# Kernel tuning notes

Hardware: AMD Instinct MI355X
Metric: run time of the kernel (lower is better)

## Reference

```python
import jax, jax.numpy as jnp
import numpy as np

B, T, D, H, FC = 32768, 7, 40, 64, 32


def lstm_layer(x_seq, W_ih, W_hh, b_ih, b_hh):
    # x_seq: [T, B, Din]; weights in PyTorch layout: W_ih [4H, Din], W_hh [4H, H]
    # Precompute the input contribution to all gates outside the scan.
    gx_seq = jnp.einsum('tbd,gd->tbg', x_seq, W_ih) + b_ih + b_hh  # [T, B, 4H]
    h0 = jnp.zeros((x_seq.shape[1], W_hh.shape[1]), x_seq.dtype)
    c0 = jnp.zeros_like(h0)

    def step(carry, gx):
        h, c = carry
        g = gx + h @ W_hh.T                      # [B, 4H]
        i, f, gg, o = jnp.split(g, 4, axis=-1)   # PyTorch gate order: i, f, g, o
        i = jax.nn.sigmoid(i)
        f = jax.nn.sigmoid(f)
        gg = jnp.tanh(gg)
        o = jax.nn.sigmoid(o)
        c = f * c + i * gg
        h = o * jnp.tanh(c)
        return (h, c), h

    (_, _), hs = jax.lax.scan(step, (h0, c0), gx_seq)
    return hs  # [T, B, H]


def setup_inputs() -> dict:
    key = jax.random.key(0)
    ks = jax.random.split(key, 13)
    s_in = 1.0 / np.sqrt(H)
    u = lambda k, shape: jax.random.uniform(k, shape, jnp.float32, -s_in, s_in)
    return {
        'x': jax.random.normal(ks[0], (B, T, D), jnp.float32),
        'W_ih0': u(ks[1], (4 * H, D)),
        'W_hh0': u(ks[2], (4 * H, H)),
        'b_ih0': u(ks[3], (4 * H,)),
        'b_hh0': u(ks[4], (4 * H,)),
        'W_ih1': u(ks[5], (4 * H, H)),
        'W_hh1': u(ks[6], (4 * H, H)),
        'b_ih1': u(ks[7], (4 * H,)),
        'b_hh1': u(ks[8], (4 * H,)),
        'W1': u(ks[9], (FC, H)),
        'b1': u(ks[10], (FC,)),
        'W2': u(ks[11], (1, FC)),
        'b2': u(ks[12], (1,)),
    }


def reference(x, W_ih0, W_hh0, b_ih0, b_hh0, W_ih1, W_hh1, b_ih1, b_hh1, W1, b1, W2, b2):
    xs = jnp.transpose(x, (1, 0, 2))                    # [T, B, D]
    h1 = lstm_layer(xs, W_ih0, W_hh0, b_ih0, b_hh0)     # [T, B, H]
    h2 = lstm_layer(h1, W_ih1, W_hh1, b_ih1, b_hh1)     # [T, B, H]
    last = h2[-1]                                       # out[:, -1, :] -> [B, H]
    # dropout is identity in eval mode
    hid = jax.nn.relu(last @ W1.T + b1)                 # [B, 32]
    return hid @ W2.T + b2                              # [B, 1]
```

## Files before the change

kernel.cpp:

```cpp
#include <hip/hip_runtime.h>

#define TT 7
#define DD 40
#define HH 64
#define RB 128
#define NRT 8
#define NTH 512
#define HS 72
#define XP 44
#define L2E 1.44269504088896340736f

typedef _Float16 f16x8 __attribute__((ext_vector_type(8)));
typedef float f32x4 __attribute__((ext_vector_type(4)));

#define MFMA(acc, a, b) acc = __builtin_amdgcn_mfma_f32_16x16x32_f16(a, b, acc, 0, 0, 0)

__device__ __forceinline__ float fast_rcp(float x) { return __builtin_amdgcn_rcpf(x); }
__device__ __forceinline__ float ex2(float x) { return __builtin_amdgcn_exp2f(x); }

__device__ __forceinline__ float lstm_hc(float a0, float a1, float a2, float a3,
                                         float &c) {
  float A = ex2(-a0);
  float E = ex2(a2);
  float F = ex2(-a1);
  float O = ex2(-a3);
  float igg = (E - 1.f) * fast_rcp((1.f + A) * (1.f + E));
  float fg  = fast_rcp(1.f + F);
  c = fg * c + igg;
  float C = ex2(c * (2.f * L2E));
  return (C - 1.f) * fast_rcp((1.f + O) * (1.f + C));
}

typedef __attribute__((address_space(3))) unsigned lds_u32_t;
typedef const __attribute__((address_space(1))) unsigned glb_u32_t;
__device__ __forceinline__ void gl_lds16(const void* g, void* l) {
  __builtin_amdgcn_global_load_lds((glb_u32_t*)g, (lds_u32_t*)l, 16, 0, 0);
}

__device__ __forceinline__ f16x8 zf() {
  f16x8 r;
  #pragma unroll
  for (int i = 0; i < 8; ++i) r[i] = (_Float16)0.f;
  return r;
}
__device__ __forceinline__ f16x8 cvt8s(const float* p, float s) {
  float4 a = *(const float4*)p, b = *(const float4*)(p + 4);
  f16x8 r;
  r[0] = (_Float16)(a.x * s); r[1] = (_Float16)(a.y * s);
  r[2] = (_Float16)(a.z * s); r[3] = (_Float16)(a.w * s);
  r[4] = (_Float16)(b.x * s); r[5] = (_Float16)(b.y * s);
  r[6] = (_Float16)(b.z * s); r[7] = (_Float16)(b.w * s);
  return r;
}
__device__ __forceinline__ f16x8 cvt8(const float* p) {
  float4 a = *(const float4*)p, b = *(const float4*)(p + 4);
  f16x8 r;
  r[0] = (_Float16)a.x; r[1] = (_Float16)a.y; r[2] = (_Float16)a.z; r[3] = (_Float16)a.w;
  r[4] = (_Float16)b.x; r[5] = (_Float16)b.y; r[6] = (_Float16)b.z; r[7] = (_Float16)b.w;
  return r;
}
__device__ __forceinline__ f16x8 pk8(float4 a, float4 b) {
  f16x8 r;
  auto p0 = __builtin_amdgcn_cvt_pkrtz(a.x, a.y);
  auto p1 = __builtin_amdgcn_cvt_pkrtz(a.z, a.w);
  auto p2 = __builtin_amdgcn_cvt_pkrtz(b.x, b.y);
  auto p3 = __builtin_amdgcn_cvt_pkrtz(b.z, b.w);
  r[0] = p0[0]; r[1] = p0[1]; r[2] = p1[0]; r[3] = p1[1];
  r[4] = p2[0]; r[5] = p2[1]; r[6] = p3[0]; r[7] = p3[1];
  return r;
}

__global__ __launch_bounds__(NTH, 2) void lstm2_r16_kernel(
    const float* __restrict__ x,
    const float* __restrict__ Wih0, const float* __restrict__ Whh0,
    const float* __restrict__ bih0, const float* __restrict__ bhh0,
    const float* __restrict__ Wih1, const float* __restrict__ Whh1,
    const float* __restrict__ bih1, const float* __restrict__ bhh1,
    const float* __restrict__ W1, const float* __restrict__ b1,
    const float* __restrict__ W2, const float* __restrict__ b2,
    float* __restrict__ out)
{
  __shared__ __align__(16) unsigned short s_h[4][RB * HS];
  __shared__ __align__(16) float s_x[2][RB * XP];

  const int tid = threadIdx.x;
  const int l   = tid & 63;
  const int wv  = tid >> 6;
  const bool L0 = (wv < 4);
  const int l15 = l & 15;
  const int lg  = l >> 4;
  const int jj  = (wv & 3) * 16 + l15;
  const int k0l = lg * 8;
  const int blk = blockIdx.x;
  const float* xg = x + (size_t)blk * RB * (TT * DD);

  const int c0 = tid, c1 = 512 + tid, c2 = 1024 + tid;
  const int r0 = c0 / 11, p0 = c0 - r0 * 11;
  const int r1 = c1 / 11, p1 = c1 - r1 * 11;
  const int r2 = c2 / 11, p2 = c2 - r2 * 11;
  const bool v0 = (p0 < 10), v1 = (p1 < 10), v2 = (c2 < 1408) && (p2 < 10);
  const float* xs0 = xg + r0 * (TT * DD) + p0 * 4;
  const float* xs1 = xg + r1 * (TT * DD) + p1 * 4;
  const float* xs2 = xg + r2 * (TT * DD) + p2 * 4;
  const int d0 = wv * 256, d1 = 2048 + wv * 256, d2 = 4096 + wv * 256;

  if (v0) gl_lds16(xs0, &s_x[0][d0]);
  if (v1) gl_lds16(xs1, &s_x[0][d1]);
  if (v2) gl_lds16(xs2, &s_x[0][d2]);

  f16x8 W[16];
  float biasv[4];
  if (L0) {
    #pragma unroll
    for (int g = 0; g < 4; ++g) {
      const float gs = (g == 2) ? 2.f * L2E : L2E;
      int n = g * 64 + jj;
      W[g]      = cvt8s(&Wih0[n * DD + k0l], gs);
      W[4 + g]  = (lg == 0) ? cvt8s(&Wih0[n * DD + 32], gs) : zf();
      W[8 + g]  = cvt8s(&Whh0[n * HH + k0l], gs);
      W[12 + g] = cvt8s(&Whh0[n * HH + 32 + k0l], gs);
      biasv[g] = (bih0[n] + bhh0[n]) * gs;
    }
  } else {
    #pragma unroll
    for (int g = 0; g < 4; ++g) {
      const float gs = (g == 2) ? 2.f * L2E : L2E;
      int n = g * 64 + jj;
      W[g]      = cvt8s(&Wih1[n * HH + k0l], gs);
      W[4 + g]  = cvt8s(&Wih1[n * HH + 32 + k0l], gs);
      W[8 + g]  = cvt8s(&Whh1[n * HH + k0l], gs);
      W[12 + g] = cvt8s(&Whh1[n * HH + 32 + k0l], gs);
      biasv[g] = (bih1[n] + bhh1[n]) * gs;
    }
  }

  float cst[NRT][4];
  #pragma unroll
  for (int rt = 0; rt < NRT; ++rt)
    #pragma unroll
    for (int r = 0; r < 4; ++r) cst[rt][r] = 0.f;

  __syncthreads();

  #pragma unroll 1
  for (int s = 0; s < TT; ++s) {
    if (s) __syncthreads();
    if (s < TT - 1) {
      float* xd = &s_x[(s + 1) & 1][0];
      const int so = (s + 1) * DD;
      if (v0) gl_lds16(xs0 + so, xd + d0);
      if (v1) gl_lds16(xs1 + so, xd + d1);
      if (v2) gl_lds16(xs2 + so, xd + d2);
    }
    const int p1r = (s - 1) & 1;

    if (L0) {
      const float* xb = &s_x[s & 1][0];
      #pragma unroll
      for (int rt = 0; rt < NRT; ++rt) {
        const float* xr = xb + (rt * 16 + l15) * XP;
        f16x8 xh = pk8(*(const float4*)(xr + k0l), *(const float4*)(xr + k0l + 4));
        f16x8 xm = xh;
        if (lg == 0) xm = pk8(*(const float4*)(xr + 32), *(const float4*)(xr + 36));

        f32x4 acc[4];
        #pragma unroll
        for (int g = 0; g < 4; ++g)
          acc[g] = (f32x4){biasv[g], biasv[g], biasv[g], biasv[g]};

        __builtin_amdgcn_s_setprio(1);
        #pragma unroll
        for (int g = 0; g < 4; ++g) MFMA(acc[g], xh, W[g]);
        #pragma unroll
        for (int g = 0; g < 4; ++g) MFMA(acc[g], xm, W[4 + g]);
        if (s) {
          const unsigned short* hp = &s_h[p1r][(rt * 16 + l15) * HS + k0l];
          f16x8 h1a = *(const f16x8*)hp;
          f16x8 h1b = *(const f16x8*)(hp + 32);
          #pragma unroll
          for (int g = 0; g < 4; ++g) MFMA(acc[g], h1a, W[8 + g]);
          #pragma unroll
          for (int g = 0; g < 4; ++g) MFMA(acc[g], h1b, W[12 + g]);
        }
        __builtin_amdgcn_s_setprio(0);

        #pragma unroll
        for (int r = 0; r < 4; ++r) {
          float h = lstm_hc(acc[0][r], acc[1][r], acc[2][r], acc[3][r], cst[rt][r]);
          s_h[s & 1][(rt * 16 + lg * 4 + r) * HS + jj] =
              __builtin_bit_cast(unsigned short, (_Float16)h);
        }
      }
    } else if (s) {
      #pragma unroll
      for (int rt = 0; rt < NRT; ++rt) {
        const unsigned short* hp = &s_h[p1r][(rt * 16 + l15) * HS + k0l];
        f16x8 h1a = *(const f16x8*)hp;
        f16x8 h1b = *(const f16x8*)(hp + 32);

        f32x4 acc[4];
        #pragma unroll
        for (int g = 0; g < 4; ++g)
          acc[g] = (f32x4){biasv[g], biasv[g], biasv[g], biasv[g]};

        __builtin_amdgcn_s_setprio(1);
        #pragma unroll
        for (int g = 0; g < 4; ++g) MFMA(acc[g], h1a, W[g]);
        #pragma unroll
        for (int g = 0; g < 4; ++g) MFMA(acc[g], h1b, W[4 + g]);
        if (s >= 2) {
          const unsigned short* qp = &s_h[2 + (s & 1)][(rt * 16 + l15) * HS + k0l];
          f16x8 q0 = *(const f16x8*)qp;
          f16x8 q1 = *(const f16x8*)(qp + 32);
          #pragma unroll
          for (int g = 0; g < 4; ++g) MFMA(acc[g], q0, W[8 + g]);
          #pragma unroll
          for (int g = 0; g < 4; ++g) MFMA(acc[g], q1, W[12 + g]);
        }
        __builtin_amdgcn_s_setprio(0);

        #pragma unroll
        for (int r = 0; r < 4; ++r) {
          float h = lstm_hc(acc[0][r], acc[1][r], acc[2][r], acc[3][r], cst[rt][r]);
          s_h[2 + p1r][(rt * 16 + lg * 4 + r) * HS + jj] =
              __builtin_bit_cast(unsigned short, (_Float16)h);
        }
      }
    }
  }

  __syncthreads();
  if (!L0) {
    #pragma unroll
    for (int rt = 0; rt < NRT; ++rt) {
      const unsigned short* hp = &s_h[0][(rt * 16 + l15) * HS + k0l];
      f16x8 h1a = *(const f16x8*)hp;
      f16x8 h1b = *(const f16x8*)(hp + 32);
      const unsigned short* qp = &s_h[3][(rt * 16 + l15) * HS + k0l];
      f16x8 q0 = *(const f16x8*)qp;
      f16x8 q1 = *(const f16x8*)(qp + 32);
      f32x4 acc[4];
      #pragma unroll
      for (int g = 0; g < 4; ++g)
        acc[g] = (f32x4){biasv[g], biasv[g], biasv[g], biasv[g]};
      __builtin_amdgcn_s_setprio(1);
      #pragma unroll
      for (int g = 0; g < 4; ++g) MFMA(acc[g], h1a, W[g]);
      #pragma unroll
      for (int g = 0; g < 4; ++g) MFMA(acc[g], h1b, W[4 + g]);
      #pragma unroll
      for (int g = 0; g < 4; ++g) MFMA(acc[g], q0, W[8 + g]);
      #pragma unroll
      for (int g = 0; g < 4; ++g) MFMA(acc[g], q1, W[12 + g]);
      __builtin_amdgcn_s_setprio(0);
      #pragma unroll
      for (int r = 0; r < 4; ++r) {
        float h = lstm_hc(acc[0][r], acc[1][r], acc[2][r], acc[3][r], cst[rt][r]);
        s_h[1][(rt * 16 + lg * 4 + r) * HS + jj] =
            __builtin_bit_cast(unsigned short, (_Float16)h);
      }
    }
  }
  __syncthreads();

  {
    const unsigned short* ap = &s_h[1][(wv * 16 + l15) * HS + k0l];
    f16x8 A0 = *(const f16x8*)ap;
    f16x8 A1 = *(const f16x8*)(ap + 32);
    f16x8 Bf0[2], Bf1[2];
    f32x4 accf[2];
    #pragma unroll
    for (int f = 0; f < 2; ++f) {
      int n = f * 16 + l15;
      Bf0[f] = cvt8(&W1[n * 64 + k0l]);
      Bf1[f] = cvt8(&W1[n * 64 + 32 + k0l]);
      float bb = b1[n];
      accf[f] = (f32x4){bb, bb, bb, bb};
    }
    #pragma unroll
    for (int f = 0; f < 2; ++f) { MFMA(accf[f], A0, Bf0[f]); MFMA(accf[f], A1, Bf1[f]); }
    float* hid = &s_x[0][0];
    #pragma unroll
    for (int f = 0; f < 2; ++f)
      #pragma unroll
      for (int r = 0; r < 4; ++r)
        hid[(wv * 16 + lg * 4 + r) * 36 + f * 16 + l15] = fmaxf(accf[f][r], 0.f);
  }
  __syncthreads();
  if (tid < RB) {
    const float* hid = &s_x[0][0];
    float a = b2[0];
    #pragma unroll
    for (int kq = 0; kq < 8; ++kq) {
      float4 hv = *(const float4*)&hid[tid * 36 + kq * 4];
      float4 wv4 = *(const float4*)&W2[kq * 4];
      a += hv.x * wv4.x + hv.y * wv4.y + hv.z * wv4.z + hv.w * wv4.w;
    }
    out[blk * RB + tid] = a;
  }
}

extern "C" void kernel_launch(void* const* d_in, const int* in_sizes, int n_in,
                              void* d_out, int out_size, void* d_ws, size_t ws_size,
                              hipStream_t stream) {
  const float* x    = (const float*)d_in[0];
  const float* Wih0 = (const float*)d_in[1];
  const float* Whh0 = (const float*)d_in[2];
  const float* bih0 = (const float*)d_in[3];
  const float* bhh0 = (const float*)d_in[4];
  const float* Wih1 = (const float*)d_in[5];
  const float* Whh1 = (const float*)d_in[6];
  const float* bih1 = (const float*)d_in[7];
  const float* bhh1 = (const float*)d_in[8];
  const float* W1   = (const float*)d_in[9];
  const float* b1   = (const float*)d_in[10];
  const float* W2   = (const float*)d_in[11];
  const float* b2   = (const float*)d_in[12];
  float* out = (float*)d_out;

  const int Btot = in_sizes[0] / (TT * DD);
  dim3 grid(Btot / RB), block(NTH);
  lstm2_r16_kernel<<<grid, block, 0, stream>>>(
      x, Wih0, Whh0, bih0, bhh0, Wih1, Whh1, bih1, bhh1, W1, b1, W2, b2, out);
}
```

Before: 56.36 us.

## Double block to 1024 threads, splitting each layer's rows across two wave groups

Doubles the block size from 512 to 1024 threads. Each LSTM layer now uses 8 waves instead of 4, and each wave handles 4 row tiles instead of 8, split by a row-half index. The x staging loads and the final FC stage are redistributed to match the new wave count. The aim is to shorten the serial per-step work of each wave and expose more parallelism. In exchange, the launch bound drops to one block per CU, and barrier and synchronisation cost grows with the larger block.

```diff
diff --git a/kernel.cpp b/kernel.cpp
--- a/kernel.cpp
+++ b/kernel.cpp
@@ -4,8 +4,8 @@
 #define DD 40
 #define HH 64
 #define RB 128
-#define NRT 8
-#define NTH 512
+#define NRT 4
+#define NTH 1024
 #define HS 72
 #define XP 44
 #define L2E 1.44269504088896340736f
@@ -70,7 +70,7 @@
   return r;
 }
 
-__global__ __launch_bounds__(NTH, 2) void lstm2_r16_kernel(
+__global__ __launch_bounds__(NTH, 1) void lstm2_r18_kernel(
     const float* __restrict__ x,
     const float* __restrict__ Wih0, const float* __restrict__ Whh0,
     const float* __restrict__ bih0, const float* __restrict__ bhh0,
@@ -86,27 +86,27 @@
   const int tid = threadIdx.x;
   const int l   = tid & 63;
   const int wv  = tid >> 6;
-  const bool L0 = (wv < 4);
+  const bool L0 = (wv < 8);
+  const int wq  = wv & 3;
+  const int wm  = (wv >> 2) & 1;
   const int l15 = l & 15;
   const int lg  = l >> 4;
-  const int jj  = (wv & 3) * 16 + l15;
+  const int jj  = wq * 16 + l15;
   const int k0l = lg * 8;
   const int blk = blockIdx.x;
   const float* xg = x + (size_t)blk * RB * (TT * DD);
 
-  const int c0 = tid, c1 = 512 + tid, c2 = 1024 + tid;
+  const int c0 = tid, c1 = 1024 + tid;
   const int r0 = c0 / 11, p0 = c0 - r0 * 11;
   const int r1 = c1 / 11, p1 = c1 - r1 * 11;
-  const int r2 = c2 / 11, p2 = c2 - r2 * 11;
-  const bool v0 = (p0 < 10), v1 = (p1 < 10), v2 = (c2 < 1408) && (p2 < 10);
+  const bool v0 = (p0 < 10);
+  const bool v1 = (c1 < 1408) && (p1 < 10);
   const float* xs0 = xg + r0 * (TT * DD) + p0 * 4;
   const float* xs1 = xg + r1 * (TT * DD) + p1 * 4;
-  const float* xs2 = xg + r2 * (TT * DD) + p2 * 4;
-  const int d0 = wv * 256, d1 = 2048 + wv * 256, d2 = 4096 + wv * 256;
+  const int d0 = wv * 256, d1 = 4096 + wv * 256;
 
   if (v0) gl_lds16(xs0, &s_x[0][d0]);
   if (v1) gl_lds16(xs1, &s_x[0][d1]);
-  if (v2) gl_lds16(xs2, &s_x[0][d2]);
 
   f16x8 W[16];
   float biasv[4];
@@ -150,7 +150,6 @@
       const int so = (s + 1) * DD;
       if (v0) gl_lds16(xs0 + so, xd + d0);
       if (v1) gl_lds16(xs1 + so, xd + d1);
-      if (v2) gl_lds16(xs2 + so, xd + d2);
     }
     const int p1r = (s - 1) & 1;
 
@@ -158,7 +157,8 @@
       const float* xb = &s_x[s & 1][0];
       #pragma unroll
       for (int rt = 0; rt < NRT; ++rt) {
-        const float* xr = xb + (rt * 16 + l15) * XP;
+        const int arow = wm * 64 + rt * 16 + l15;
+        const float* xr = xb + arow * XP;
         f16x8 xh = pk8(*(const float4*)(xr + k0l), *(const float4*)(xr + k0l + 4));
         f16x8 xm = xh;
         if (lg == 0) xm = pk8(*(const float4*)(xr + 32), *(const float4*)(xr + 36));
@@ -174,7 +174,7 @@
         #pragma unroll
         for (int g = 0; g < 4; ++g) MFMA(acc[g], xm, W[4 + g]);
         if (s) {
-          const unsigned short* hp = &s_h[p1r][(rt * 16 + l15) * HS + k0l];
+          const unsigned short* hp = &s_h[p1r][arow * HS + k0l];
           f16x8 h1a = *(const f16x8*)hp;
           f16x8 h1b = *(const f16x8*)(hp + 32);
           #pragma unroll
@@ -187,14 +187,15 @@
         #pragma unroll
         for (int r = 0; r < 4; ++r) {
           float h = lstm_hc(acc[0][r], acc[1][r], acc[2][r], acc[3][r], cst[rt][r]);
-          s_h[s & 1][(rt * 16 + lg * 4 + r) * HS + jj] =
+          s_h[s & 1][(wm * 64 + rt * 16 + lg * 4 + r) * HS + jj] =
               __builtin_bit_cast(unsigned short, (_Float16)h);
         }
       }
     } else if (s) {
       #pragma unroll
       for (int rt = 0; rt < NRT; ++rt) {
-        const unsigned short* hp = &s_h[p1r][(rt * 16 + l15) * HS + k0l];
+        const int arow = wm * 64 + rt * 16 + l15;
+        const unsigned short* hp = &s_h[p1r][arow * HS + k0l];
         f16x8 h1a = *(const f16x8*)hp;
         f16x8 h1b = *(const f16x8*)(hp + 32);
 
@@ -209,7 +210,7 @@
         #pragma unroll
         for (int g = 0; g < 4; ++g) MFMA(acc[g], h1b, W[4 + g]);
         if (s >= 2) {
-          const unsigned short* qp = &s_h[2 + (s & 1)][(rt * 16 + l15) * HS + k0l];
+          const unsigned short* qp = &s_h[2 + (s & 1)][arow * HS + k0l];
           f16x8 q0 = *(const f16x8*)qp;
           f16x8 q1 = *(const f16x8*)(qp + 32);
           #pragma unroll
@@ -222,7 +223,7 @@
         #pragma unroll
         for (int r = 0; r < 4; ++r) {
           float h = lstm_hc(acc[0][r], acc[1][r], acc[2][r], acc[3][r], cst[rt][r]);
-          s_h[2 + p1r][(rt * 16 + lg * 4 + r) * HS + jj] =
+          s_h[2 + p1r][(wm * 64 + rt * 16 + lg * 4 + r) * HS + jj] =
               __builtin_bit_cast(unsigned short, (_Float16)h);
         }
       }
@@ -233,10 +234,11 @@
   if (!L0) {
     #pragma unroll
     for (int rt = 0; rt < NRT; ++rt) {
-      const unsigned short* hp = &s_h[0][(rt * 16 + l15) * HS + k0l];
+      const int arow = wm * 64 + rt * 16 + l15;
+      const unsigned short* hp = &s_h[0][arow * HS + k0l];
       f16x8 h1a = *(const f16x8*)hp;
       f16x8 h1b = *(const f16x8*)(hp + 32);
-      const unsigned short* qp = &s_h[3][(rt * 16 + l15) * HS + k0l];
+      const unsigned short* qp = &s_h[3][arow * HS + k0l];
       f16x8 q0 = *(const f16x8*)qp;
       f16x8 q1 = *(const f16x8*)(qp + 32);
       f32x4 acc[4];
@@ -256,7 +258,7 @@
       #pragma unroll
       for (int r = 0; r < 4; ++r) {
         float h = lstm_hc(acc[0][r], acc[1][r], acc[2][r], acc[3][r], cst[rt][r]);
-        s_h[1][(rt * 16 + lg * 4 + r) * HS + jj] =
+        s_h[1][(wm * 64 + rt * 16 + lg * 4 + r) * HS + jj] =
             __builtin_bit_cast(unsigned short, (_Float16)h);
       }
     }
@@ -264,27 +266,22 @@
   __syncthreads();
 
   {
-    const unsigned short* ap = &s_h[1][(wv * 16 + l15) * HS + k0l];
+    const int twv = wv >> 1;
+    const int fh  = wv & 1;
+    const unsigned short* ap = &s_h[1][(twv * 16 + l15) * HS + k0l];
     f16x8 A0 = *(const f16x8*)ap;
     f16x8 A1 = *(const f16x8*)(ap + 32);
-    f16x8 Bf0[2], Bf1[2];
-    f32x4 accf[2];
-    #pragma unroll
-    for (int f = 0; f < 2; ++f) {
-      int n = f * 16 + l15;
-      Bf0[f] = cvt8(&W1[n * 64 + k0l]);
-      Bf1[f] = cvt8(&W1[n * 64 + 32 + k0l]);
-      float bb = b1[n];
-      accf[f] = (f32x4){bb, bb, bb, bb};
-    }
-    #pragma unroll
-    for (int f = 0; f < 2; ++f) { MFMA(accf[f], A0, Bf0[f]); MFMA(accf[f], A1, Bf1[f]); }
+    int n = fh * 16 + l15;
+    f16x8 Bf0 = cvt8(&W1[n * 64 + k0l]);
+    f16x8 Bf1 = cvt8(&W1[n * 64 + 32 + k0l]);
+    float bb = b1[n];
+    f32x4 accf = (f32x4){bb, bb, bb, bb};
+    MFMA(accf, A0, Bf0);
+    MFMA(accf, A1, Bf1);
     float* hid = &s_x[0][0];
     #pragma unroll
-    for (int f = 0; f < 2; ++f)
-      #pragma unroll
-      for (int r = 0; r < 4; ++r)
-        hid[(wv * 16 + lg * 4 + r) * 36 + f * 16 + l15] = fmaxf(accf[f][r], 0.f);
+    for (int r = 0; r < 4; ++r)
+      hid[(twv * 16 + lg * 4 + r) * 36 + fh * 16 + l15] = fmaxf(accf[r], 0.f);
   }
   __syncthreads();
   if (tid < RB) {
@@ -320,6 +317,6 @@
 
   const int Btot = in_sizes[0] / (TT * DD);
   dim3 grid(Btot / RB), block(NTH);
-  lstm2_r16_kernel<<<grid, block, 0, stream>>>(
+  lstm2_r18_kernel<<<grid, block, 0, stream>>>(
       x, Wih0, Whh0, bih0, bhh0, Wih1, Whh1, bih1, bhh1, W1, b1, W2, b2, out);
 }
```

Result: slower. 76.90 us (+36.4%).
